# Optimization experiments

Hardware: AMD Instinct MI355X
Metric: run time of the kernel (lower is better)

Reference implementation:

```python
import jax, jax.numpy as jnp
import numpy as np

HIDDEN = 1024
HEADS = 16
HEAD = HIDDEN // HEADS


def setup_inputs() -> dict:
    key = jax.random.key(0)
    ks = jax.random.split(key, 10)
    B, T, N = 4, 1024, 1024
    x = jax.random.normal(ks[0], (B, T, HIDDEN), dtype=jnp.float32)
    encoder_feature = jax.random.normal(ks[1], (B, N, HIDDEN), dtype=jnp.float32)
    s = 1.0 / np.sqrt(HIDDEN)
    Wq = jax.random.normal(ks[2], (HIDDEN, HIDDEN), dtype=jnp.float32) * s
    bq = jax.random.normal(ks[3], (HIDDEN,), dtype=jnp.float32) * 0.02
    Wk = jax.random.normal(ks[4], (HIDDEN, HIDDEN), dtype=jnp.float32) * s
    bk = jax.random.normal(ks[5], (HIDDEN,), dtype=jnp.float32) * 0.02
    Wv = jax.random.normal(ks[6], (HIDDEN, HIDDEN), dtype=jnp.float32) * s
    bv = jax.random.normal(ks[7], (HIDDEN,), dtype=jnp.float32) * 0.02
    return {"x": x, "encoder_feature": encoder_feature,
            "Wq": Wq, "bq": bq, "Wk": Wk, "bk": bk, "Wv": Wv, "bv": bv}


def reference(x, encoder_feature, Wq, bq, Wk, bk, Wv, bv):
    B, T, _ = x.shape
    N = encoder_feature.shape[1]
    # torch Linear: y = x @ W.T + b
    q = (x @ Wq.T + bq).reshape(B, T, HEADS, HEAD)
    k = (encoder_feature @ Wk.T + bk).reshape(B, N, HEADS, HEAD)
    v = (encoder_feature @ Wv.T + bv).reshape(B, N, HEADS, HEAD)
    att = jnp.einsum('bthd,bnhd->bhtn', q, k) / jnp.sqrt(jnp.float32(HEAD))
    # causal tril mask sliced to (T, N): position t attends to n <= t
    mask = jnp.tril(jnp.ones((T, N), dtype=bool))
    att = jnp.where(mask[None, None], att, jnp.finfo(att.dtype).min)
    att = jax.nn.softmax(att, axis=-1)
    out = jnp.einsum('bhtn,bnhd->bthd', att, v).reshape(B, T, HIDDEN)
    # NOTE: original forward never applies out_proj; dropout=0.0 (identity)
    return out
```

## Files before the change

### kernel.cpp

```cpp
#include <hip/hip_runtime.h>
#include <hip/hip_bf16.h>
#include <cstdint>
#include <cstddef>

#define B_SZ 4
#define T_SZ 1024
#define N_SZ 1024
#define HID 1024
#define NHEADS 16
#define DHEAD 64

typedef __bf16 bf16x8 __attribute__((ext_vector_type(8)));
typedef __bf16 bf16x4 __attribute__((ext_vector_type(4)));
typedef float floatx4 __attribute__((ext_vector_type(4)));

#define LDT 72
#define LKV 72
#define LP  72

#define SM_SCALE_LOG2E 0.18033688011112042f

__device__ __forceinline__ void async_copy16(const void* gsrc, void* ldst) {
    __builtin_amdgcn_global_load_lds(
        (const __attribute__((address_space(1))) void*)(uintptr_t)gsrc,
        (__attribute__((address_space(3))) void*)(uintptr_t)ldst, 16, 0, 0);
}

__global__ __launch_bounds__(256)
void cvt5_f32_bf16(const float* __restrict__ x, const float* __restrict__ enc,
                   const float* __restrict__ wq, const float* __restrict__ wk,
                   const float* __restrict__ wv,
                   __bf16* __restrict__ xb, __bf16* __restrict__ eb,
                   __bf16* __restrict__ wqb, __bf16* __restrict__ wkb,
                   __bf16* __restrict__ wvb)
{
#pragma unroll
    for (int c = 0; c < 8; ++c) {
        const int chunk = blockIdx.x * 8 + c;
        const float* s; __bf16* d; int base;
        if (chunk < 2048)      { s = x;   d = xb;  base = chunk; }
        else if (chunk < 4096) { s = enc; d = eb;  base = chunk - 2048; }
        else if (chunk < 4608) { s = wq;  d = wqb; base = chunk - 4096; }
        else if (chunk < 5120) { s = wk;  d = wkb; base = chunk - 4608; }
        else                   { s = wv;  d = wvb; base = chunk - 5120; }
        const size_t off = (size_t)base * 2048 + (size_t)threadIdx.x * 8;
        const float4 a = *(const float4*)(s + off);
        const float4 b = *(const float4*)(s + off + 4);
        bf16x8 o;
        o[0] = (__bf16)a.x; o[1] = (__bf16)a.y; o[2] = (__bf16)a.z; o[3] = (__bf16)a.w;
        o[4] = (__bf16)b.x; o[5] = (__bf16)b.y; o[6] = (__bf16)b.z; o[7] = (__bf16)b.w;
        *(bf16x8*)(d + off) = o;
    }
}

__global__ __launch_bounds__(256)
void gemm3_bt_bias(const __bf16* __restrict__ xb, const __bf16* __restrict__ eb,
                   const __bf16* __restrict__ wqb, const __bf16* __restrict__ wkb,
                   const __bf16* __restrict__ wvb,
                   const float* __restrict__ bq, const float* __restrict__ bk,
                   const float* __restrict__ bv,
                   __bf16* __restrict__ qo, __bf16* __restrict__ ko,
                   __bf16* __restrict__ vo)
{
    constexpr int K = HID;
    __shared__ __align__(16) __bf16 As[128 * 64];
    __shared__ __align__(16) __bf16 Bs[128 * 64];

    const int bid  = blockIdx.x;
    const int xcd  = bid & 7;
    const int slot = bid >> 3;
    const int bn   = (slot & 7) * 128;
    const int pair = xcd * 12 + (slot >> 3);
    const int z    = pair >> 5;
    const int bm   = (pair & 31) * 128;

    const __bf16* A; const __bf16* W; const float* bias; __bf16* C;
    if (z == 0)      { A = xb; W = wqb; bias = bq; C = qo; }
    else if (z == 1) { A = eb; W = wkb; bias = bk; C = ko; }
    else             { A = eb; W = wvb; bias = bv; C = vo; }

    const int tid  = threadIdx.x;
    const int wave = tid >> 6;
    const int lane = tid & 63;
    const int l15  = lane & 15;
    const int quad = lane >> 4;
    const int wm = (wave >> 1) * 64;
    const int wn = (wave & 1) * 64;

    floatx4 acc[4][4];
#pragma unroll
    for (int i = 0; i < 4; ++i)
#pragma unroll
        for (int j = 0; j < 4; ++j)
            acc[i][j] = (floatx4)(0.0f);

    const int sr = tid >> 3;
    const int sc = (((tid & 7) ^ (sr & 7))) * 8;

    for (int k0 = 0; k0 < K; k0 += 64) {
#pragma unroll
        for (int p = 0; p < 4; ++p) {
            const int r = p * 32 + sr;
            async_copy16(A + (size_t)(bm + r) * K + k0 + sc,
                         (char*)As + p * 4096 + tid * 16);
            async_copy16(W + (size_t)(bn + r) * K + k0 + sc,
                         (char*)Bs + p * 4096 + tid * 16);
        }
        __syncthreads();
#pragma unroll
        for (int kk = 0; kk < 2; ++kk) {
            const int ch = kk * 4 + quad;
            bf16x8 af[4], bfr[4];
#pragma unroll
            for (int i = 0; i < 4; ++i) {
                const int ra = wm + i * 16 + l15;
                const int rb = wn + i * 16 + l15;
                af[i]  = *(const bf16x8*)((const char*)As + ra * 128 + ((ch ^ (ra & 7)) << 4));
                bfr[i] = *(const bf16x8*)((const char*)Bs + rb * 128 + ((ch ^ (rb & 7)) << 4));
            }
#pragma unroll
            for (int mi = 0; mi < 4; ++mi)
#pragma unroll
                for (int ni = 0; ni < 4; ++ni)
                    acc[mi][ni] = __builtin_amdgcn_mfma_f32_16x16x32_bf16(
                        af[mi], bfr[ni], acc[mi][ni], 0, 0, 0);
        }
        __syncthreads();
    }

    const int crow0 = bm + wm + quad * 4;
    const int ccol0 = bn + wn + l15;
#pragma unroll
    for (int ni = 0; ni < 4; ++ni) {
        const int n = ccol0 + ni * 16;
        const float bias_f = bias[n];
#pragma unroll
        for (int mi = 0; mi < 4; ++mi) {
#pragma unroll
            for (int r = 0; r < 4; ++r) {
                const int m = crow0 + mi * 16 + r;
                C[(size_t)m * HID + n] = (__bf16)(acc[mi][ni][r] + bias_f);
            }
        }
    }
}

__global__ __launch_bounds__(256)
void gemm_bt_bias_f32in(const float* __restrict__ A,
                        const float* __restrict__ W,
                        const float* __restrict__ bias,
                        __hip_bfloat16* __restrict__ C)
{
    constexpr int K = HID;
    __shared__ __align__(16) __hip_bfloat16 As[128 * LDT];
    __shared__ __align__(16) __hip_bfloat16 Bs[128 * LDT];

    const int tid  = threadIdx.x;
    const int wave = tid >> 6;
    const int lane = tid & 63;
    const int bm = blockIdx.y * 128;
    const int bn = blockIdx.x * 128;
    const int wm = (wave >> 1) * 64;
    const int wn = (wave & 1) * 64;

    floatx4 acc[4][4];
#pragma unroll
    for (int i = 0; i < 4; ++i)
#pragma unroll
        for (int j = 0; j < 4; ++j)
            acc[i][j] = (floatx4)(0.0f);

    const int lr = tid >> 4;
    const int lc = (tid & 15) * 4;

    for (int k0 = 0; k0 < K; k0 += 64) {
#pragma unroll
        for (int qq = 0; qq < 8; ++qq) {
            const int r = lr + qq * 16;
            const float4 a4 = *(const float4*)(A + (size_t)(bm + r) * K + k0 + lc);
            const float4 w4 = *(const float4*)(W + (size_t)(bn + r) * K + k0 + lc);
            bf16x4 av, wv;
            av[0] = (__bf16)a4.x; av[1] = (__bf16)a4.y; av[2] = (__bf16)a4.z; av[3] = (__bf16)a4.w;
            wv[0] = (__bf16)w4.x; wv[1] = (__bf16)w4.y; wv[2] = (__bf16)w4.z; wv[3] = (__bf16)w4.w;
            *(bf16x4*)(As + r * LDT + lc) = av;
            *(bf16x4*)(Bs + r * LDT + lc) = wv;
        }
        __syncthreads();
#pragma unroll
        for (int kk = 0; kk < 2; ++kk) {
            const int krow = kk * 32 + (lane >> 4) * 8;
            const int mrow = wm + (lane & 15);
            const int nrow = wn + (lane & 15);
            bf16x8 af[4], bfr[4];
#pragma unroll
            for (int i = 0; i < 4; ++i) {
                af[i]  = *(const bf16x8*)(As + (mrow + i * 16) * LDT + krow);
                bfr[i] = *(const bf16x8*)(Bs + (nrow + i * 16) * LDT + krow);
            }
#pragma unroll
            for (int mi = 0; mi < 4; ++mi)
#pragma unroll
                for (int ni = 0; ni < 4; ++ni)
                    acc[mi][ni] = __builtin_amdgcn_mfma_f32_16x16x32_bf16(
                        af[mi], bfr[ni], acc[mi][ni], 0, 0, 0);
        }
        __syncthreads();
    }

    const int crow0 = bm + wm + (lane >> 4) * 4;
    const int ccol0 = bn + wn + (lane & 15);
#pragma unroll
    for (int ni = 0; ni < 4; ++ni) {
        const int n = ccol0 + ni * 16;
        const float bias_f = bias[n];
#pragma unroll
        for (int mi = 0; mi < 4; ++mi) {
#pragma unroll
            for (int r = 0; r < 4; ++r) {
                const int m = crow0 + mi * 16 + r;
                C[(size_t)m * HID + n] = __float2bfloat16(acc[mi][ni][r] + bias_f);
            }
        }
    }
}

__global__ __launch_bounds__(256)
void attn_flash_mfma_v4(const __bf16* __restrict__ q,
                        const __bf16* __restrict__ k,
                        const __bf16* __restrict__ v,
                        float* __restrict__ out)
{
    __shared__ __align__(16) __bf16 Ks[2][64 * LKV];
    __shared__ __align__(16) __bf16 Vt[2][64 * LKV];
    __shared__ __align__(16) __bf16 Ps[4][32 * LP];

    const int tid  = threadIdx.x;
    const int wave = tid >> 6;
    const int lane = tid & 63;
    const int l15  = lane & 15;
    const int quad = lane >> 4;

    const int bx = blockIdx.x;
    const int jj = bx & 7;
    const int bt = ((bx >> 8) & 1) ? jj : 7 - jj;
    const int bh = bx >> 3;
    const int h  = bh & (NHEADS - 1);
    const int b  = bh >> 4;
    const int t0 = bt * 128;

    const __bf16* kbase = k + (size_t)b * N_SZ * HID + h * DHEAD;
    const __bf16* vbase = v + (size_t)b * N_SZ * HID + h * DHEAD;

    bf16x8 qf[2][2];
    {
        const __bf16* qb = q + (size_t)(b * T_SZ + t0 + wave * 32) * HID + h * DHEAD;
#pragma unroll
        for (int g = 0; g < 2; ++g)
#pragma unroll
            for (int kk = 0; kk < 2; ++kk) {
                const bf16x8 raw = *(const bf16x8*)(qb + (size_t)(g * 16 + l15) * HID
                                                    + kk * 32 + quad * 8);
#pragma unroll
                for (int j = 0; j < 8; ++j)
                    qf[g][kk][j] = (__bf16)((float)raw[j] * SM_SCALE_LOG2E);
            }
    }

    const int kr = tid >> 3;
    const int kc = (tid & 7) * 8;
    const int vn = tid & 63;
    const int vd = (tid >> 6) * 8;

#pragma unroll
    for (int p = 0; p < 2; ++p) {
        *(bf16x8*)(&Ks[0][(kr + p * 32) * LKV + kc]) =
            *(const bf16x8*)(kbase + (size_t)(kr + p * 32) * HID + kc);
        const bf16x8 vv = *(const bf16x8*)(vbase + (size_t)vn * HID + vd + p * 32);
#pragma unroll
        for (int j = 0; j < 8; ++j)
            Vt[0][(vd + p * 32 + j) * LKV + vn] = vv[j];
    }
    __syncthreads();

    float lsum[2] = {0.f, 0.f};
    floatx4 oacc[2][4];
#pragma unroll
    for (int g = 0; g < 2; ++g)
#pragma unroll
        for (int nd = 0; nd < 4; ++nd) oacc[g][nd] = (floatx4)(0.0f);

    __bf16* pw = &Ps[wave][0];
    const int ntiles = 2 * bt + 2;

    for (int it = 0; it < ntiles; ++it) {
        const int bi = it & 1;
        const int n0 = it * 64;

        bf16x8 nk0, nk1, nv0, nv1;
        const bool pf = (it + 1 < ntiles);
        if (pf) {
            const int nn0 = n0 + 64;
            nk0 = *(const bf16x8*)(kbase + (size_t)(nn0 + kr) * HID + kc);
            nk1 = *(const bf16x8*)(kbase + (size_t)(nn0 + kr + 32) * HID + kc);
            nv0 = *(const bf16x8*)(vbase + (size_t)(nn0 + vn) * HID + vd);
            nv1 = *(const bf16x8*)(vbase + (size_t)(nn0 + vn) * HID + vd + 32);
        }

        floatx4 st[2][4];
#pragma unroll
        for (int g = 0; g < 2; ++g)
#pragma unroll
            for (int ni = 0; ni < 4; ++ni) st[g][ni] = (floatx4)(0.0f);
        const __bf16* ksb = &Ks[bi][0];
#pragma unroll
        for (int kk = 0; kk < 2; ++kk) {
            const int ko = kk * 32 + quad * 8;
#pragma unroll
            for (int ni = 0; ni < 4; ++ni) {
                const bf16x8 af = *(const bf16x8*)(ksb + (ni * 16 + l15) * LKV + ko);
                st[0][ni] = __builtin_amdgcn_mfma_f32_16x16x32_bf16(af, qf[0][kk], st[0][ni], 0, 0, 0);
                st[1][ni] = __builtin_amdgcn_mfma_f32_16x16x32_bf16(af, qf[1][kk], st[1][ni], 0, 0, 0);
            }
        }

        const bool msk = (it >= 2 * bt);
#pragma unroll
        for (int g = 0; g < 2; ++g) {
            const int tq = t0 + wave * 32 + g * 16 + l15;
#pragma unroll
            for (int ni = 0; ni < 4; ++ni) {
                bf16x4 pk;
#pragma unroll
                for (int r = 0; r < 4; ++r) {
                    float p = exp2f(st[g][ni][r]);
                    if (msk) {
                        const int nn = n0 + ni * 16 + quad * 4 + r;
                        p = (nn > tq) ? 0.f : p;
                    }
                    lsum[g] += p;
                    pk[r] = (__bf16)p;
                }
                *(bf16x4*)(pw + (g * 16 + l15) * LP + ni * 16 + quad * 4) = pk;
            }
        }

        const __bf16* vtb = &Vt[bi][0];
#pragma unroll
        for (int kk = 0; kk < 2; ++kk) {
            const int ko = kk * 32 + quad * 8;
            const bf16x8 bp0 = *(const bf16x8*)(pw + l15 * LP + ko);
            const bf16x8 bp1 = *(const bf16x8*)(pw + (16 + l15) * LP + ko);
#pragma unroll
            for (int nd = 0; nd < 4; ++nd) {
                const bf16x8 av = *(const bf16x8*)(vtb + (nd * 16 + l15) * LKV + ko);
                oacc[0][nd] = __builtin_amdgcn_mfma_f32_16x16x32_bf16(av, bp0, oacc[0][nd], 0, 0, 0);
                oacc[1][nd] = __builtin_amdgcn_mfma_f32_16x16x32_bf16(av, bp1, oacc[1][nd], 0, 0, 0);
            }
        }

        if (pf) {
            const int wb = bi ^ 1;
            *(bf16x8*)(&Ks[wb][kr * LKV + kc]) = nk0;
            *(bf16x8*)(&Ks[wb][(kr + 32) * LKV + kc]) = nk1;
#pragma unroll
            for (int j = 0; j < 8; ++j) {
                Vt[wb][(vd + j) * LKV + vn] = nv0[j];
                Vt[wb][(vd + 32 + j) * LKV + vn] = nv1[j];
            }
        }
        __syncthreads();
    }

#pragma unroll
    for (int g = 0; g < 2; ++g) {
        lsum[g] += __shfl_xor(lsum[g], 16, 64);
        lsum[g] += __shfl_xor(lsum[g], 32, 64);
    }
#pragma unroll
    for (int g = 0; g < 2; ++g) {
        const float invl = 1.0f / lsum[g];
        const int trow = t0 + wave * 32 + g * 16 + l15;
        float* ob = out + (size_t)(b * T_SZ + trow) * HID + h * DHEAD + quad * 4;
#pragma unroll
        for (int nd = 0; nd < 4; ++nd) {
            float4 o4;
            o4.x = oacc[g][nd][0] * invl;
            o4.y = oacc[g][nd][1] * invl;
            o4.z = oacc[g][nd][2] * invl;
            o4.w = oacc[g][nd][3] * invl;
            *(float4*)(ob + nd * 16) = o4;
        }
    }
}

extern "C" void kernel_launch(void* const* d_in, const int* in_sizes, int n_in,
                              void* d_out, int out_size, void* d_ws, size_t ws_size,
                              hipStream_t stream) {
    const float* x   = (const float*)d_in[0];
    const float* enc = (const float*)d_in[1];
    const float* Wq  = (const float*)d_in[2];
    const float* bq  = (const float*)d_in[3];
    const float* Wk  = (const float*)d_in[4];
    const float* bk  = (const float*)d_in[5];
    const float* Wv  = (const float*)d_in[6];
    const float* bv  = (const float*)d_in[7];
    float* out = (float*)d_out;

    char* ws = (char*)d_ws;
    const size_t MiB = 1024 * 1024;
    __bf16* q_ws = (__bf16*)(ws);
    __bf16* k_ws = (__bf16*)(ws + 8 * MiB);
    __bf16* v_ws = (__bf16*)(ws + 16 * MiB);

    const dim3 blk(256);
    if (ws_size >= 46 * MiB) {
        __bf16* xb  = (__bf16*)(ws + 24 * MiB);
        __bf16* eb  = (__bf16*)(ws + 32 * MiB);
        __bf16* wqb = (__bf16*)(ws + 40 * MiB);
        __bf16* wkb = (__bf16*)(ws + 42 * MiB);
        __bf16* wvb = (__bf16*)(ws + 44 * MiB);
        cvt5_f32_bf16<<<dim3(704), blk, 0, stream>>>(x, enc, Wq, Wk, Wv,
                                                     xb, eb, wqb, wkb, wvb);
        gemm3_bt_bias<<<dim3(768), blk, 0, stream>>>(
            xb, eb, wqb, wkb, wvb, bq, bk, bv, q_ws, k_ws, v_ws);
    } else {
        const dim3 gg(HID / 128, (B_SZ * T_SZ) / 128);
        gemm_bt_bias_f32in<<<gg, blk, 0, stream>>>(x,   Wq, bq, (__hip_bfloat16*)q_ws);
        gemm_bt_bias_f32in<<<gg, blk, 0, stream>>>(enc, Wk, bk, (__hip_bfloat16*)k_ws);
        gemm_bt_bias_f32in<<<gg, blk, 0, stream>>>(enc, Wv, bv, (__hip_bfloat16*)v_ws);
    }

    attn_flash_mfma_v4<<<dim3(512), blk, 0, stream>>>(q_ws, k_ws, v_ws, out);
}
```

Baseline: 171.4 us.

## Replace QKV projection GEMM with 256x256-tile 8-phase pipelined kernel

Replaces the 128x128-tile, single-buffered QKV projection GEMM with a 256x256-tile kernel using 512 threads, double-buffered LDS split into halves, and an 8-phase schedule. Global-to-LDS async loads for later K tiles are interleaved with MFMA quadrants, using explicit barriers, vmcnt waits and setprio. The goal is to hide global load latency, cut the per-tile barrier stalls of the old kernel and raise operand reuse. The cost is far fewer blocks (192 over the GPU's CUs), a larger LDS footprint (128 KB per block) and fragile hand-written wait counts.

New measurement: 160.8 us. 1.07x faster.

```diff
diff --git a/kernel.cpp b/kernel.cpp
--- a/kernel.cpp
+++ b/kernel.cpp
@@ -53,8 +53,45 @@
     }
 }
 
-__global__ __launch_bounds__(256)
-void gemm3_bt_bias(const __bf16* __restrict__ xb, const __bf16* __restrict__ eb,
+#define PBAR() do {                              \
+    asm volatile("" ::: "memory");               \
+    __builtin_amdgcn_s_barrier();                \
+    __builtin_amdgcn_sched_barrier(0);           \
+} while (0)
+
+#define MFMA_Q(QM, QN, BREG) do {                                             \
+    __builtin_amdgcn_s_setprio(1);                                            \
+    _Pragma("unroll")                                                         \
+    for (int mf_ = 0; mf_ < 4; ++mf_) {                                       \
+        _Pragma("unroll")                                                     \
+        for (int nf_ = 0; nf_ < 2; ++nf_) {                                   \
+            acc[QM][QN][mf_][nf_] = __builtin_amdgcn_mfma_f32_16x16x32_bf16(  \
+                a[mf_][0], BREG[nf_][0], acc[QM][QN][mf_][nf_], 0, 0, 0);     \
+            acc[QM][QN][mf_][nf_] = __builtin_amdgcn_mfma_f32_16x16x32_bf16(  \
+                a[mf_][1], BREG[nf_][1], acc[QM][QN][mf_][nf_], 0, 0, 0);     \
+        }                                                                     \
+    }                                                                         \
+    __builtin_amdgcn_s_setprio(0);                                            \
+} while (0)
+
+#define LOAD_A(BUF, HALF) do {                                                \
+    _Pragma("unroll")                                                         \
+    for (int mf_ = 0; mf_ < 4; ++mf_) {                                       \
+        a[mf_][0] = ldsA(BUF, HALF, mf_, 0);                                  \
+        a[mf_][1] = ldsA(BUF, HALF, mf_, 1);                                  \
+    }                                                                         \
+} while (0)
+
+#define LOAD_B(DST, BUF, HALF) do {                                           \
+    _Pragma("unroll")                                                         \
+    for (int nf_ = 0; nf_ < 2; ++nf_) {                                       \
+        DST[nf_][0] = ldsB(BUF, HALF, nf_, 0);                                \
+        DST[nf_][1] = ldsB(BUF, HALF, nf_, 1);                                \
+    }                                                                         \
+} while (0)
+
+__global__ __launch_bounds__(512, 2)
+void gemm3_256_8ph(const __bf16* __restrict__ xb, const __bf16* __restrict__ eb,
                    const __bf16* __restrict__ wqb, const __bf16* __restrict__ wkb,
                    const __bf16* __restrict__ wvb,
                    const float* __restrict__ bq, const float* __restrict__ bk,
@@ -62,17 +99,16 @@
                    __bf16* __restrict__ qo, __bf16* __restrict__ ko,
                    __bf16* __restrict__ vo)
 {
-    constexpr int K = HID;
-    __shared__ __align__(16) __bf16 As[128 * 64];
-    __shared__ __align__(16) __bf16 Bs[128 * 64];
-
-    const int bid  = blockIdx.x;
-    const int xcd  = bid & 7;
-    const int slot = bid >> 3;
-    const int bn   = (slot & 7) * 128;
-    const int pair = xcd * 12 + (slot >> 3);
-    const int z    = pair >> 5;
-    const int bm   = (pair & 31) * 128;
+    __shared__ __align__(16) __bf16 AS[2][2][8192];
+    __shared__ __align__(16) __bf16 BS[2][2][8192];
+
+    const int bid = blockIdx.x;
+    const int swz = (bid & 7) * 24 + (bid >> 3);
+    const int mt  = swz >> 2;
+    const int nt  = swz & 3;
+    const int z   = mt >> 4;
+    const int bm  = (mt & 15) << 8;
+    const int bn  = nt << 8;
 
     const __bf16* A; const __bf16* W; const float* bias; __bf16* C;
     if (z == 0)      { A = xb; W = wqb; bias = bq; C = qo; }
@@ -80,70 +116,130 @@
     else             { A = eb; W = wvb; bias = bv; C = vo; }
 
     const int tid  = threadIdx.x;
-    const int wave = tid >> 6;
     const int lane = tid & 63;
+    const int wid  = tid >> 6;
     const int l15  = lane & 15;
     const int quad = lane >> 4;
-    const int wm = (wave >> 1) * 64;
-    const int wn = (wave & 1) * 64;
-
-    floatx4 acc[4][4];
-#pragma unroll
-    for (int i = 0; i < 4; ++i)
-#pragma unroll
-        for (int j = 0; j < 4; ++j)
-            acc[i][j] = (floatx4)(0.0f);
-
-    const int sr = tid >> 3;
-    const int sc = (((tid & 7) ^ (sr & 7))) * 8;
-
-    for (int k0 = 0; k0 < K; k0 += 64) {
-#pragma unroll
-        for (int p = 0; p < 4; ++p) {
-            const int r = p * 32 + sr;
-            async_copy16(A + (size_t)(bm + r) * K + k0 + sc,
-                         (char*)As + p * 4096 + tid * 16);
-            async_copy16(W + (size_t)(bn + r) * K + k0 + sc,
-                         (char*)Bs + p * 4096 + tid * 16);
-        }
-        __syncthreads();
-#pragma unroll
-        for (int kk = 0; kk < 2; ++kk) {
-            const int ch = kk * 4 + quad;
-            bf16x8 af[4], bfr[4];
-#pragma unroll
-            for (int i = 0; i < 4; ++i) {
-                const int ra = wm + i * 16 + l15;
-                const int rb = wn + i * 16 + l15;
-                af[i]  = *(const bf16x8*)((const char*)As + ra * 128 + ((ch ^ (ra & 7)) << 4));
-                bfr[i] = *(const bf16x8*)((const char*)Bs + rb * 128 + ((ch ^ (rb & 7)) << 4));
-            }
-#pragma unroll
-            for (int mi = 0; mi < 4; ++mi)
-#pragma unroll
-                for (int ni = 0; ni < 4; ++ni)
-                    acc[mi][ni] = __builtin_amdgcn_mfma_f32_16x16x32_bf16(
-                        af[mi], bfr[ni], acc[mi][ni], 0, 0, 0);
-        }
-        __syncthreads();
-    }
-
-    const int crow0 = bm + wm + quad * 4;
-    const int ccol0 = bn + wn + l15;
-#pragma unroll
-    for (int ni = 0; ni < 4; ++ni) {
-        const int n = ccol0 + ni * 16;
-        const float bias_f = bias[n];
-#pragma unroll
-        for (int mi = 0; mi < 4; ++mi) {
-#pragma unroll
-            for (int r = 0; r < 4; ++r) {
-                const int m = crow0 + mi * 16 + r;
-                C[(size_t)m * HID + n] = (__bf16)(acc[mi][ni][r] + bias_f);
-            }
-        }
-    }
+    const int wmid = wid >> 2;
+    const int wnid = wid & 3;
+
+    const int sr  = tid >> 3;
+    const int sch = tid & 7;
+
+    auto stage2 = [&](const __bf16* src, __bf16* dst, int gRow0, int kt) {
+        const int c = (sch ^ (sr & 7)) << 3;
+        async_copy16(src + (size_t)(gRow0 + sr) * HID + kt * 64 + c,
+                     (char*)dst + tid * 16);
+        async_copy16(src + (size_t)(gRow0 + sr + 64) * HID + kt * 64 + c,
+                     (char*)dst + 8192 + tid * 16);
+    };
+
+    auto ldsA = [&](int buf, int half, int mf, int kk) -> bf16x8 {
+        const int r = wmid * 64 + mf * 16 + l15;
+        return *(const bf16x8*)((const char*)&AS[buf][half][0] + r * 128 +
+                                (((kk * 4 + quad) ^ (r & 7)) << 4));
+    };
+    auto ldsB = [&](int buf, int half, int nf, int kk) -> bf16x8 {
+        const int r = wnid * 32 + nf * 16 + l15;
+        return *(const bf16x8*)((const char*)&BS[buf][half][0] + r * 128 +
+                                (((kk * 4 + quad) ^ (r & 7)) << 4));
+    };
+
+    bf16x8 a[4][2], b0[2][2], b1[2][2];
+    floatx4 acc[2][2][4][2];
+#pragma unroll
+    for (int i = 0; i < 2; ++i)
+#pragma unroll
+        for (int j = 0; j < 2; ++j)
+#pragma unroll
+            for (int m = 0; m < 4; ++m)
+#pragma unroll
+                for (int n = 0; n < 2; ++n)
+                    acc[i][j][m][n] = (floatx4)(0.0f);
+
+    stage2(A, &AS[0][0][0], bm,       0);
+    stage2(W, &BS[0][0][0], bn,       0);
+    stage2(W, &BS[0][1][0], bn + 128, 0);
+    stage2(A, &AS[0][1][0], bm + 128, 0);
+    stage2(A, &AS[1][0][0], bm,       1);
+    stage2(W, &BS[1][0][0], bn,       1);
+    stage2(W, &BS[1][1][0], bn + 128, 1);
+    asm volatile("s_waitcnt vmcnt(6)" ::: "memory");
+    PBAR();
+
+#pragma unroll 1
+    for (int it = 0; it < 8; ++it) {
+        const int kt1 = 2 * it + 1;
+        const int kta = (it < 7) ? 2 * it + 2 : 14;
+        const int ktb = (it < 7) ? 2 * it + 3 : 15;
+
+        LOAD_A(0, 0);
+        LOAD_B(b0, 0, 0);
+        stage2(A, &AS[1][1][0], bm + 128, kt1);
+        PBAR();
+        MFMA_Q(0, 0, b0);
+        PBAR();
+        LOAD_B(b1, 0, 1);
+        stage2(A, &AS[0][0][0], bm, kta);
+        PBAR();
+        MFMA_Q(0, 1, b1);
+        PBAR();
+        LOAD_A(0, 1);
+        stage2(W, &BS[0][0][0], bn, kta);
+        PBAR();
+        MFMA_Q(1, 1, b1);
+        PBAR();
+        stage2(W, &BS[0][1][0], bn + 128, kta);
+        PBAR();
+        MFMA_Q(1, 0, b0);
+        asm volatile("s_waitcnt vmcnt(6)" ::: "memory");
+        PBAR();
+        LOAD_A(1, 0);
+        LOAD_B(b0, 1, 0);
+        stage2(A, &AS[0][1][0], bm + 128, kta);
+        PBAR();
+        MFMA_Q(0, 0, b0);
+        PBAR();
+        LOAD_B(b1, 1, 1);
+        stage2(A, &AS[1][0][0], bm, ktb);
+        PBAR();
+        MFMA_Q(0, 1, b1);
+        PBAR();
+        LOAD_A(1, 1);
+        stage2(W, &BS[1][0][0], bn, ktb);
+        PBAR();
+        MFMA_Q(1, 1, b1);
+        PBAR();
+        stage2(W, &BS[1][1][0], bn + 128, ktb);
+        PBAR();
+        MFMA_Q(1, 0, b0);
+        asm volatile("s_waitcnt vmcnt(6)" ::: "memory");
+        PBAR();
+    }
+
+#pragma unroll
+    for (int qn = 0; qn < 2; ++qn)
+#pragma unroll
+        for (int nf = 0; nf < 2; ++nf) {
+            const int n = bn + qn * 128 + wnid * 32 + nf * 16 + l15;
+            const float bias_f = bias[n];
+#pragma unroll
+            for (int qm = 0; qm < 2; ++qm)
+#pragma unroll
+                for (int mf = 0; mf < 4; ++mf) {
+                    const int m0 = bm + qm * 128 + wmid * 64 + mf * 16 + quad * 4;
+#pragma unroll
+                    for (int r = 0; r < 4; ++r)
+                        C[(size_t)(m0 + r) * HID + n] =
+                            (__bf16)(acc[qm][qn][mf][nf][r] + bias_f);
+                }
+        }
 }
+
+#undef LOAD_A
+#undef LOAD_B
+#undef MFMA_Q
+#undef PBAR
 
 __global__ __launch_bounds__(256)
 void gemm_bt_bias_f32in(const float* __restrict__ A,
@@ -421,7 +517,7 @@
         __bf16* wvb = (__bf16*)(ws + 44 * MiB);
         cvt5_f32_bf16<<<dim3(704), blk, 0, stream>>>(x, enc, Wq, Wk, Wv,
                                                      xb, eb, wqb, wkb, wvb);
-        gemm3_bt_bias<<<dim3(768), blk, 0, stream>>>(
+        gemm3_256_8ph<<<dim3(192), dim3(512), 0, stream>>>(
             xb, eb, wqb, wkb, wvb, bq, bk, bv, q_ws, k_ws, v_ws);
     } else {
         const dim3 gg(HID / 128, (B_SZ * T_SZ) / 128);
```
